# Optimization experiments

Measured on AMD Instinct MI355X. Metric: run time of the kernel, lower is better.

Reference implementation:

```python
import jax, jax.numpy as jnp
import numpy as np

NUM_HEADS = 16
HEAD_DIM = 64  # hidden_size 1024 / 16 heads


def setup_inputs() -> dict:
    key = jax.random.key(0)
    k1, k2 = jax.random.split(key)
    B, S, D = 2, 2048, 1024
    hidden_states = jax.random.normal(k1, (B, S, D), dtype=jnp.float32)
    # fast_qkv: bias-free fused qkv projection + separate q/v biases (init zeros in torch)
    W_qkv = jax.random.normal(k2, (D, 3 * D), dtype=jnp.float32) * (1.0 / np.sqrt(D))
    q_bias = jnp.zeros((D,), dtype=jnp.float32)
    v_bias = jnp.zeros((D,), dtype=jnp.float32)
    return {"hidden_states": hidden_states, "W_qkv": W_qkv, "q_bias": q_bias, "v_bias": v_bias}


def reference(hidden_states, W_qkv, q_bias, v_bias):
    B, S, D = hidden_states.shape
    H, hd = NUM_HEADS, HEAD_DIM
    qkv = hidden_states @ W_qkv                      # (B,S,3D)
    q, k, v = jnp.split(qkv, 3, axis=-1)
    q = q + q_bias
    v = v + v_bias
    # (B,S,H,hd)
    q = q.reshape(B, S, H, hd)
    k = k.reshape(B, S, H, hd)
    v = v.reshape(B, S, H, hd)
    q = q / jnp.sqrt(jnp.asarray(hd, dtype=q.dtype))
    # full (B,H,S,S) score tensor, softmax in fp32 then cast back (matches torch)
    scores = jnp.einsum('bqhd,bkhd->bhqk', q, k)
    probs = jax.nn.softmax(scores.astype(jnp.float32), axis=-1).astype(v.dtype)
    ctx = jnp.einsum('bhqk,bkhd->bqhd', probs, v)    # (B,S,H,hd)
    return ctx.reshape(B, S, D)
```

## Files before the change

### kernel.cpp

```cpp
#include <hip/hip_runtime.h>
#include <hip/hip_bf16.h>

typedef _Float16 half_t;
typedef _Float16 h8 __attribute__((ext_vector_type(8)));
typedef _Float16 h4 __attribute__((ext_vector_type(4)));
typedef _Float16 h2 __attribute__((ext_vector_type(2)));
typedef float f32x4 __attribute__((ext_vector_type(4)));
typedef float f4 __attribute__((ext_vector_type(4)));

#define DEVI __device__ __forceinline__

constexpr int NB = 2;
constexpr int S  = 2048;
constexpr int DM = 1024;
constexpr int NH = 16;
constexpr int HD = 64;
constexpr long M = (long)NB * S;
constexpr int N3 = 3 * DM;

DEVI f32x4 mfma16(h8 a, h8 b, f32x4 c) {
  return __builtin_amdgcn_mfma_f32_16x16x32_f16(a, b, c, 0, 0, 0);
}
DEVI f32x4 mfma16h(h4 a, h4 b, f32x4 c) {
  return __builtin_amdgcn_mfma_f32_16x16x16f16(a, b, c, 0, 0, 0);
}
DEVI h8 ld8h(const half_t* p) { return *(const h8*)p; }

#if __has_builtin(__builtin_amdgcn_exp2f)
DEVI float ex2(float x) { return __builtin_amdgcn_exp2f(x); }
#else
DEVI float ex2(float x) { float r; asm("v_exp_f32 %0, %1" : "=v"(r) : "v"(x)); return r; }
#endif

DEVI h2 pk2(float a, float b) {
  auto r = __builtin_amdgcn_cvt_pkrtz(a, b);
  h2 o; __builtin_memcpy(&o, &r, sizeof(o)); return o;
}

DEVI void gl_lds16(const half_t* g, half_t* l) {
  __builtin_amdgcn_global_load_lds(
      (const __attribute__((address_space(1))) void*)g,
      (__attribute__((address_space(3))) void*)l, 16, 0, 0);
}

__global__ void prep(const float* __restrict__ hidden, half_t* __restrict__ Hb,
                     const float* __restrict__ W, half_t* __restrict__ Wt) {
  __shared__ float tile[32][33];
  const int id = blockIdx.x, t = threadIdx.x;
  if (id < 2048) {
    const long i = ((long)id * 256 + t) * 8;
    const f4 a = *(const f4*)(hidden + i), b = *(const f4*)(hidden + i + 4);
    h8 r;
    #pragma unroll
    for (int k = 0; k < 4; k++) { r[k] = (half_t)a[k]; r[4 + k] = (half_t)b[k]; }
    *(h8*)(Hb + i) = r;
  } else {
    const int id2 = id - 2048;
    const int c0 = (id2 % 96) * 32, r0 = (id2 / 96) * 32;
    const int x = t & 31, y = t >> 5;
    #pragma unroll
    for (int i = 0; i < 32; i += 8) tile[y + i][x] = W[(long)(r0 + y + i) * N3 + c0 + x];
    __syncthreads();
    #pragma unroll
    for (int i = 0; i < 32; i += 8)
      Wt[(long)(c0 + y + i) * DM + r0 + x] = (half_t)tile[x][y + i];
  }
}

__global__ __launch_bounds__(256) void qkv_gemm(
    const half_t* __restrict__ A, const half_t* __restrict__ Bt,
    const float* __restrict__ qbias, const float* __restrict__ vbias,
    half_t* __restrict__ Qf, half_t* __restrict__ Kf, half_t* __restrict__ Vt)
{
  constexpr int BM = 128, BN = 128, BK = 32;
  __shared__ alignas(16) half_t As[BM * BK];
  __shared__ alignas(16) half_t Bs[BN * BK];
  const int t = threadIdx.x, lane = t & 63, wave = t >> 6;
  const int quad = lane >> 4, l16 = lane & 15;
  const int id = blockIdx.x, xcd = id & 7, jj = id >> 3;
  const int m0 = (xcd * 4 + (jj & 3)) * BM;
  const int n0 = (jj >> 2) * BN;
  const int wm = (wave & 1) * 64, wn = (wave >> 1) * 64;

  const half_t* aP0 = A  + (long)(m0 + (t >> 2)) * DM + (t & 3) * 8;
  const half_t* aP1 = aP0 + (long)64 * DM;
  const half_t* bP0 = Bt + (long)(n0 + (t >> 2)) * DM + (t & 3) * 8;
  const half_t* bP1 = bP0 + (long)64 * DM;
  half_t* asW = As + wave * 512;
  half_t* bsW = Bs + wave * 512;

  f32x4 acc[4][4] = {};

  for (int k0 = 0; k0 < DM; k0 += BK) {
    __syncthreads();
    gl_lds16(aP0 + k0, asW);
    gl_lds16(aP1 + k0, asW + 2048);
    gl_lds16(bP0 + k0, bsW);
    gl_lds16(bP1 + k0, bsW + 2048);
    __builtin_amdgcn_s_waitcnt(0);
    __syncthreads();

    h8 af[4], bfr[4];
    #pragma unroll
    for (int i = 0; i < 4; i++) af[i]  = ld8h(&As[(wm + i * 16 + l16) * BK + quad * 8]);
    #pragma unroll
    for (int j = 0; j < 4; j++) bfr[j] = ld8h(&Bs[(wn + j * 16 + l16) * BK + quad * 8]);
    #pragma unroll
    for (int i = 0; i < 4; i++)
      #pragma unroll
      for (int j = 0; j < 4; j++)
        acc[i][j] = mfma16(af[i], bfr[j], acc[i][j]);
  }

  if (n0 < 2 * DM) {
    #pragma unroll
    for (int i = 0; i < 4; i++) {
      #pragma unroll
      for (int j = 0; j < 4; j++) {
        const int n = n0 + wn + j * 16 + l16;
        #pragma unroll
        for (int r = 0; r < 4; r++) {
          const long m = m0 + wm + i * 16 + quad * 4 + r;
          const float cv = acc[i][j][r];
          if (n < DM) {
            Qf[m * DM + n] = (half_t)((cv + qbias[n]) * 0.1803368801f);
          } else {
            Kf[m * DM + (n - DM)] = (half_t)cv;
          }
        }
      }
    }
  } else {
    const int dBase = n0 + wn - 2 * DM;
    #pragma unroll
    for (int i = 0; i < 4; i++) {
      const long mb = m0 + wm + i * 16 + quad * 4;
      const int bb = (int)(mb >> 11);
      const int ss = (int)(mb & (S - 1));
      #pragma unroll
      for (int j = 0; j < 4; j++) {
        const int dd = dBase + j * 16 + l16;
        const float vb4 = vbias[dd];
        h4 vv;
        #pragma unroll
        for (int r = 0; r < 4; r++) vv[r] = (half_t)(acc[i][j][r] + vb4);
        *(h4*)&Vt[(((long)bb * NH + (dd >> 6)) * HD + (dd & 63)) * S + ss] = vv;
      }
    }
  }
}

__global__ __launch_bounds__(512) void attn(
    const half_t* __restrict__ Qf, const half_t* __restrict__ Kf,
    const half_t* __restrict__ Vt, float* __restrict__ out)
{
  constexpr int LK = 72, LV = 72;
  __shared__ alignas(16) half_t smem[2 * 64 * LK + 2 * 64 * LV];
  half_t* const KsB = smem;
  half_t* const VsB = smem + 2 * 64 * LK;

  const int bh = blockIdx.y, b = bh >> 4, h = bh & 15;
  const int qt = blockIdx.x;
  const int t = threadIdx.x, lane = t & 63, wave = t >> 6;
  const int w4 = wave & 3, kvh = wave >> 2;
  const int quad = lane >> 4, l16 = lane & 15;

  const long qrow0 = (long)b * S + qt * 128 + w4 * 32;
  const half_t* qg = Qf + qrow0 * DM + h * HD;
  const long kb0 = (long)kvh * (S / 2);
  const half_t* kg = Kf + ((long)b * S + kb0) * DM + h * HD;
  const half_t* vg = Vt + (long)bh * HD * S + kb0;

  h8 bq[2][2];
  #pragma unroll
  for (int qi = 0; qi < 2; qi++)
    #pragma unroll
    for (int dh = 0; dh < 2; dh++)
      bq[qi][dh] = ld8h(&qg[(long)(qi * 16 + l16) * DM + dh * 32 + quad * 8]);

  const int tg = t & 255;
  const int r0s = tg >> 3, c0s = (tg & 7) * 8;
  const int r1s = 32 + r0s;
  half_t* const ksW = KsB + kvh * (64 * LK);
  half_t* const vsW = VsB + kvh * (64 * LV);
  h8 kreg[2], vreg[2];
  kreg[0] = ld8h(&kg[(long)r0s * DM + c0s]);
  kreg[1] = ld8h(&kg[(long)r1s * DM + c0s]);
  vreg[0] = ld8h(&vg[(long)r0s * S + c0s]);
  vreg[1] = ld8h(&vg[(long)r1s * S + c0s]);

  const f32x4 z4 = {0.f, 0.f, 0.f, 0.f};
  const h4 vones = {(half_t)1.f, (half_t)1.f, (half_t)1.f, (half_t)1.f};

  f32x4 O[2][4] = {};
  f32x4 lacc[2] = {};

  constexpr int NT = (S / 2) / 64;
  for (int kt = 0; kt < NT; ++kt) {
    __syncthreads();
    *(h8*)&ksW[r0s * LK + c0s] = kreg[0];
    *(h8*)&ksW[r1s * LK + c0s] = kreg[1];
    *(h8*)&vsW[r0s * LV + c0s] = vreg[0];
    *(h8*)&vsW[r1s * LV + c0s] = vreg[1];
    __syncthreads();

    if (kt < NT - 1) {
      const long ko = (long)(kt + 1) * 64;
      kreg[0] = ld8h(&kg[(ko + r0s) * DM + c0s]);
      kreg[1] = ld8h(&kg[(ko + r1s) * DM + c0s]);
      vreg[0] = ld8h(&vg[(long)r0s * S + ko + c0s]);
      vreg[1] = ld8h(&vg[(long)r1s * S + ko + c0s]);
    }

    h4 pa[2][4];
    #pragma unroll
    for (int g = 0; g < 4; g++) {
      const h8 kf0 = ld8h(&ksW[(g * 16 + l16) * LK + quad * 8]);
      const h8 kf1 = ld8h(&ksW[(g * 16 + l16) * LK + 32 + quad * 8]);
      #pragma unroll
      for (int qi = 0; qi < 2; qi++) {
        f32x4 sc = mfma16(kf0, bq[qi][0], z4);
        sc = mfma16(kf1, bq[qi][1], sc);
        const h2 lo = pk2(ex2(sc[0]), ex2(sc[1]));
        const h2 hi = pk2(ex2(sc[2]), ex2(sc[3]));
        union { h4 v; h2 p[2]; } u; u.p[0] = lo; u.p[1] = hi;
        pa[qi][g] = u.v;
      }
    }

    #pragma unroll
    for (int g = 0; g < 4; g++) {
      lacc[0] = mfma16h(pa[0][g], vones, lacc[0]);
      lacc[1] = mfma16h(pa[1][g], vones, lacc[1]);
    }

    #pragma unroll
    for (int j = 0; j < 4; j++) {
      #pragma unroll
      for (int g = 0; g < 4; g++) {
        const h4 vf = *(const h4*)&vsW[(j * 16 + l16) * LV + g * 16 + quad * 4];
        O[0][j] = mfma16h(pa[0][g], vf, O[0][j]);
        O[1][j] = mfma16h(pa[1][g], vf, O[1][j]);
      }
    }
  }

  __syncthreads();
  float* const xb = (float*)smem;
  float* const xl = xb + 8192;
  if (kvh) {
    #pragma unroll
    for (int qi = 0; qi < 2; qi++) {
      #pragma unroll
      for (int j = 0; j < 4; j++)
        *(f4*)&xb[(((w4 * 2 + qi) * 4 + j) * 64 + lane) * 4] = O[qi][j];
      if (l16 == 0) {
        #pragma unroll
        for (int r = 0; r < 4; r++)
          xl[(w4 * 2 + qi) * 16 + quad * 4 + r] = lacc[qi][r];
      }
    }
  }
  __syncthreads();
  if (!kvh) {
    #pragma unroll
    for (int qi = 0; qi < 2; qi++) {
      #pragma unroll
      for (int j = 0; j < 4; j++)
        O[qi][j] += *(const f4*)&xb[(((w4 * 2 + qi) * 4 + j) * 64 + lane) * 4];
      #pragma unroll
      for (int r = 0; r < 4; r++) {
        const float linv = 1.f / (lacc[qi][r] + xl[(w4 * 2 + qi) * 16 + quad * 4 + r]);
        const long srow = qrow0 + qi * 16 + quad * 4 + r;
        #pragma unroll
        for (int j = 0; j < 4; j++)
          out[srow * DM + h * HD + j * 16 + l16] = O[qi][j][r] * linv;
      }
    }
  }
}

extern "C" void kernel_launch(void* const* d_in, const int* in_sizes, int n_in,
                              void* d_out, int out_size, void* d_ws, size_t ws_size,
                              hipStream_t stream) {
  (void)in_sizes; (void)n_in; (void)out_size; (void)ws_size;
  const float* hidden = (const float*)d_in[0];
  const float* W      = (const float*)d_in[1];
  const float* qbias  = (const float*)d_in[2];
  const float* vbias  = (const float*)d_in[3];
  float* out = (float*)d_out;

  half_t* ws = (half_t*)d_ws;
  half_t* Hb = ws;
  half_t* Wt = Hb + M * DM;
  half_t* Qf = Wt + (long)N3 * DM;
  half_t* Kf = Qf + M * DM;
  half_t* Vt = Kf + M * DM;

  prep<<<2048 + 3072, 256, 0, stream>>>(hidden, Hb, W, Wt);
  qkv_gemm<<<(N3 / 128) * (int)(M / 128), 256, 0, stream>>>(Hb, Wt, qbias, vbias, Qf, Kf, Vt);
  attn<<<dim3(S / 128, NB * NH), 512, 0, stream>>>(Qf, Kf, Vt, out);
}
```

Measured before the change: 171.0 us.

## Double-buffer K/V LDS tiles in attention and stage V-transpose stores through LDS

The attention kernel now keeps two LDS buffers for K and V. Each iteration writes the next tile while computing on the current one, which cuts the per-iteration barriers from two to one and prefetches two tiles ahead. The QKV GEMM epilogue for V transposes the output through shared memory so each thread writes contiguous 16-byte chunks along S, instead of scattered 8-byte stores. The cost is double the attention LDS footprint, which may reduce occupancy, plus extra barriers in the GEMM epilogue.

```diff
diff --git a/kernel.cpp b/kernel.cpp
--- a/kernel.cpp
+++ b/kernel.cpp
@@ -73,8 +73,10 @@
     half_t* __restrict__ Qf, half_t* __restrict__ Kf, half_t* __restrict__ Vt)
 {
   constexpr int BM = 128, BN = 128, BK = 32;
-  __shared__ alignas(16) half_t As[BM * BK];
-  __shared__ alignas(16) half_t Bs[BN * BK];
+  constexpr int TL = 136;
+  __shared__ alignas(16) half_t smem[64 * TL];
+  half_t* const As = smem;
+  half_t* const Bs = smem + 4096;
   const int t = threadIdx.x, lane = t & 63, wave = t >> 6;
   const int quad = lane >> 4, l16 = lane & 15;
   const int id = blockIdx.x, xcd = id & 7, jj = id >> 3;
@@ -131,21 +133,36 @@
       }
     }
   } else {
-    const int dBase = n0 + wn - 2 * DM;
-    #pragma unroll
-    for (int i = 0; i < 4; i++) {
-      const long mb = m0 + wm + i * 16 + quad * 4;
-      const int bb = (int)(mb >> 11);
-      const int ss = (int)(mb & (S - 1));
-      #pragma unroll
-      for (int j = 0; j < 4; j++) {
-        const int dd = dBase + j * 16 + l16;
-        const float vb4 = vbias[dd];
-        h4 vv;
-        #pragma unroll
-        for (int r = 0; r < 4; r++) vv[r] = (half_t)(acc[i][j][r] + vb4);
-        *(h4*)&Vt[(((long)bb * NH + (dd >> 6)) * HD + (dd & 63)) * S + ss] = vv;
-      }
+    const int bb = (int)((long)m0 >> 11);
+    const int s0 = m0 & (S - 1);
+    __syncthreads();
+    #pragma unroll
+    for (int hp = 0; hp < 2; hp++) {
+      if ((wave >> 1) == hp) {
+        #pragma unroll
+        for (int j = 0; j < 4; j++) {
+          const int dl = j * 16 + l16;
+          const float vb = vbias[(n0 - 2 * DM) + hp * 64 + dl];
+          #pragma unroll
+          for (int i = 0; i < 4; i++) {
+            const int ml = wm + i * 16 + quad * 4;
+            h4 vv;
+            #pragma unroll
+            for (int r = 0; r < 4; r++) vv[r] = (half_t)(acc[i][j][r] + vb);
+            *(h4*)&smem[dl * TL + ml] = vv;
+          }
+        }
+      }
+      __syncthreads();
+      {
+        const int dl = t >> 2, mc = (t & 3) * 32;
+        const int dd = (n0 - 2 * DM) + hp * 64 + dl;
+        half_t* dst = &Vt[(((long)bb * NH + (dd >> 6)) * HD + (dd & 63)) * S + s0 + mc];
+        const half_t* src = &smem[dl * TL + mc];
+        #pragma unroll
+        for (int k = 0; k < 4; k++) *(h8*)(dst + k * 8) = ld8h(src + k * 8);
+      }
+      if (hp == 0) __syncthreads();
     }
   }
 }
@@ -155,9 +172,9 @@
     const half_t* __restrict__ Vt, float* __restrict__ out)
 {
   constexpr int LK = 72, LV = 72;
-  __shared__ alignas(16) half_t smem[2 * 64 * LK + 2 * 64 * LV];
+  __shared__ alignas(16) half_t smem[4 * 64 * LK + 4 * 64 * LV];
   half_t* const KsB = smem;
-  half_t* const VsB = smem + 2 * 64 * LK;
+  half_t* const VsB = smem + 4 * 64 * LK;
 
   const int bh = blockIdx.y, b = bh >> 4, h = bh & 15;
   const int qt = blockIdx.x;
@@ -181,13 +198,25 @@
   const int tg = t & 255;
   const int r0s = tg >> 3, c0s = (tg & 7) * 8;
   const int r1s = 32 + r0s;
-  half_t* const ksW = KsB + kvh * (64 * LK);
-  half_t* const vsW = VsB + kvh * (64 * LV);
+  half_t* const ksW0 = KsB + kvh * (64 * LK);
+  half_t* const vsW0 = VsB + kvh * (64 * LV);
+  half_t* const ksW1 = ksW0 + 2 * (64 * LK);
+  half_t* const vsW1 = vsW0 + 2 * (64 * LV);
   h8 kreg[2], vreg[2];
+
   kreg[0] = ld8h(&kg[(long)r0s * DM + c0s]);
   kreg[1] = ld8h(&kg[(long)r1s * DM + c0s]);
   vreg[0] = ld8h(&vg[(long)r0s * S + c0s]);
   vreg[1] = ld8h(&vg[(long)r1s * S + c0s]);
+  *(h8*)&ksW0[r0s * LK + c0s] = kreg[0];
+  *(h8*)&ksW0[r1s * LK + c0s] = kreg[1];
+  *(h8*)&vsW0[r0s * LV + c0s] = vreg[0];
+  *(h8*)&vsW0[r1s * LV + c0s] = vreg[1];
+  kreg[0] = ld8h(&kg[(long)(64 + r0s) * DM + c0s]);
+  kreg[1] = ld8h(&kg[(long)(64 + r1s) * DM + c0s]);
+  vreg[0] = ld8h(&vg[(long)r0s * S + 64 + c0s]);
+  vreg[1] = ld8h(&vg[(long)r1s * S + 64 + c0s]);
+  __syncthreads();
 
   const f32x4 z4 = {0.f, 0.f, 0.f, 0.f};
   const h4 vones = {(half_t)1.f, (half_t)1.f, (half_t)1.f, (half_t)1.f};
@@ -197,15 +226,20 @@
 
   constexpr int NT = (S / 2) / 64;
   for (int kt = 0; kt < NT; ++kt) {
-    __syncthreads();
-    *(h8*)&ksW[r0s * LK + c0s] = kreg[0];
-    *(h8*)&ksW[r1s * LK + c0s] = kreg[1];
-    *(h8*)&vsW[r0s * LV + c0s] = vreg[0];
-    *(h8*)&vsW[r1s * LV + c0s] = vreg[1];
-    __syncthreads();
-
-    if (kt < NT - 1) {
-      const long ko = (long)(kt + 1) * 64;
+    const int cur = kt & 1;
+    half_t* const ksN = cur ? ksW0 : ksW1;
+    half_t* const vsN = cur ? vsW0 : vsW1;
+    const half_t* const ksC = cur ? ksW1 : ksW0;
+    const half_t* const vsC = cur ? vsW1 : vsW0;
+
+    if (kt + 1 < NT) {
+      *(h8*)&ksN[r0s * LK + c0s] = kreg[0];
+      *(h8*)&ksN[r1s * LK + c0s] = kreg[1];
+      *(h8*)&vsN[r0s * LV + c0s] = vreg[0];
+      *(h8*)&vsN[r1s * LV + c0s] = vreg[1];
+    }
+    if (kt + 2 < NT) {
+      const long ko = (long)(kt + 2) * 64;
       kreg[0] = ld8h(&kg[(ko + r0s) * DM + c0s]);
       kreg[1] = ld8h(&kg[(ko + r1s) * DM + c0s]);
       vreg[0] = ld8h(&vg[(long)r0s * S + ko + c0s]);
@@ -215,8 +249,8 @@
     h4 pa[2][4];
     #pragma unroll
     for (int g = 0; g < 4; g++) {
-      const h8 kf0 = ld8h(&ksW[(g * 16 + l16) * LK + quad * 8]);
-      const h8 kf1 = ld8h(&ksW[(g * 16 + l16) * LK + 32 + quad * 8]);
+      const h8 kf0 = ld8h(&ksC[(g * 16 + l16) * LK + quad * 8]);
+      const h8 kf1 = ld8h(&ksC[(g * 16 + l16) * LK + 32 + quad * 8]);
       #pragma unroll
       for (int qi = 0; qi < 2; qi++) {
         f32x4 sc = mfma16(kf0, bq[qi][0], z4);
@@ -238,11 +272,13 @@
     for (int j = 0; j < 4; j++) {
       #pragma unroll
       for (int g = 0; g < 4; g++) {
-        const h4 vf = *(const h4*)&vsW[(j * 16 + l16) * LV + g * 16 + quad * 4];
+        const h4 vf = *(const h4*)&vsC[(j * 16 + l16) * LV + g * 16 + quad * 4];
         O[0][j] = mfma16h(pa[0][g], vf, O[0][j]);
         O[1][j] = mfma16h(pa[1][g], vf, O[1][j]);
       }
     }
+
+    __syncthreads();
   }
 
   __syncthreads();
```

New measurement: 179.4 us. 4.9% more time.

## Double-buffer LDS tiles in QKV GEMM to overlap global loads with MFMA

Applied to the files above, without the earlier changes.

Turns the QKV projection GEMM's single shared-memory tile into a two-stage ping-pong buffer. The next K-slice is issued into the alternate buffer before the current slice is read and fed to MFMA, with one barrier per iteration instead of two. The goal is to hide global-to-LDS latency behind matrix work rather than stalling on a full wait each step. It doubles LDS use per block and drops the explicit wait-count, so correctness now depends on the compiler inserting the right waits for the async LDS loads.

```diff
diff --git a/kernel.cpp b/kernel.cpp
--- a/kernel.cpp
+++ b/kernel.cpp
@@ -73,8 +73,8 @@
     half_t* __restrict__ Qf, half_t* __restrict__ Kf, half_t* __restrict__ Vt)
 {
   constexpr int BM = 128, BN = 128, BK = 32;
-  __shared__ alignas(16) half_t As[BM * BK];
-  __shared__ alignas(16) half_t Bs[BN * BK];
+  __shared__ alignas(16) half_t As[2][BM * BK];
+  __shared__ alignas(16) half_t Bs[2][BN * BK];
   const int t = threadIdx.x, lane = t & 63, wave = t >> 6;
   const int quad = lane >> 4, l16 = lane & 15;
   const int id = blockIdx.x, xcd = id & 7, jj = id >> 3;
@@ -86,30 +86,42 @@
   const half_t* aP1 = aP0 + (long)64 * DM;
   const half_t* bP0 = Bt + (long)(n0 + (t >> 2)) * DM + (t & 3) * 8;
   const half_t* bP1 = bP0 + (long)64 * DM;
-  half_t* asW = As + wave * 512;
-  half_t* bsW = Bs + wave * 512;
+  half_t* const asW0 = &As[0][wave * 512];
+  half_t* const bsW0 = &Bs[0][wave * 512];
+  half_t* const asW1 = &As[1][wave * 512];
+  half_t* const bsW1 = &Bs[1][wave * 512];
 
   f32x4 acc[4][4] = {};
 
-  for (int k0 = 0; k0 < DM; k0 += BK) {
-    __syncthreads();
-    gl_lds16(aP0 + k0, asW);
-    gl_lds16(aP1 + k0, asW + 2048);
-    gl_lds16(bP0 + k0, bsW);
-    gl_lds16(bP1 + k0, bsW + 2048);
-    __builtin_amdgcn_s_waitcnt(0);
-    __syncthreads();
+  gl_lds16(aP0, asW0);
+  gl_lds16(aP1, asW0 + 2048);
+  gl_lds16(bP0, bsW0);
+  gl_lds16(bP1, bsW0 + 2048);
+  __syncthreads();
+
+  constexpr int NKT = DM / BK;
+  for (int kt = 0; kt < NKT; ++kt) {
+    const int cur = kt & 1;
+    if (kt + 1 < NKT) {
+      const int k0 = (kt + 1) * BK;
+      gl_lds16(aP0 + k0, cur ? asW0 : asW1);
+      gl_lds16(aP1 + k0, (cur ? asW0 : asW1) + 2048);
+      gl_lds16(bP0 + k0, cur ? bsW0 : bsW1);
+      gl_lds16(bP1 + k0, (cur ? bsW0 : bsW1) + 2048);
+    }
 
     h8 af[4], bfr[4];
     #pragma unroll
-    for (int i = 0; i < 4; i++) af[i]  = ld8h(&As[(wm + i * 16 + l16) * BK + quad * 8]);
-    #pragma unroll
-    for (int j = 0; j < 4; j++) bfr[j] = ld8h(&Bs[(wn + j * 16 + l16) * BK + quad * 8]);
+    for (int i = 0; i < 4; i++) af[i]  = ld8h(&As[cur][(wm + i * 16 + l16) * BK + quad * 8]);
+    #pragma unroll
+    for (int j = 0; j < 4; j++) bfr[j] = ld8h(&Bs[cur][(wn + j * 16 + l16) * BK + quad * 8]);
     #pragma unroll
     for (int i = 0; i < 4; i++)
       #pragma unroll
       for (int j = 0; j < 4; j++)
         acc[i][j] = mfma16(af[i], bfr[j], acc[i][j]);
+
+    __syncthreads();
   }
 
   if (n0 < 2 * DM) {
```

Result: slower. 175.4 us (+2.5%).
